# Performance work log

Measured on AMD Instinct MI355X. Metric: run time of the kernel, lower is better.

Reference implementation:

```python
import jax, jax.numpy as jnp
import numpy as np

NEG_SLOPE = 0.2  # PyG GATConv default


def gat_conv(x, W, a_src, a_dst, b, src, dst, n):
    """Single-head PyG-style GATConv with self-loops already appended to (src, dst)."""
    h = x @ W                                   # [N, F]
    alpha_src = h @ a_src                       # [N]
    alpha_dst = h @ a_dst                       # [N]
    e = alpha_src[src] + alpha_dst[dst]         # [E] per-edge logit (message j->i)
    e = jax.nn.leaky_relu(e, NEG_SLOPE)
    # numerically stable softmax over edges grouped by destination node
    m = jax.ops.segment_max(e, dst, num_segments=n)
    ex = jnp.exp(e - m[dst])
    denom = jax.ops.segment_sum(ex, dst, num_segments=n)
    alpha = ex / denom[dst]                     # [E]
    out = jax.ops.segment_sum(alpha[:, None] * h[src], dst, num_segments=n)
    return out + b


def setup_inputs() -> dict:
    key = jax.random.key(0)
    ks = jax.random.split(key, 16)
    N, C, E = 50000, 128, 800000
    x = jax.random.normal(ks[0], (N, C), dtype=jnp.float32)
    edge_index = jax.random.randint(ks[1], (2, E), 0, N, dtype=jnp.int64)

    def lin(k, din, dout):
        return jax.random.normal(k, (din, dout), dtype=jnp.float32) / np.sqrt(din)

    def att(k, d):
        return jax.random.normal(k, (d,), dtype=jnp.float32) / np.sqrt(d)

    d1, d2, d3 = 2 * C, C // 2, 1
    return {
        "x": x, "edge_index": edge_index,
        "W1": lin(ks[2], C, d1), "as1": att(ks[3], d1), "ad1": att(ks[4], d1), "b1": jnp.zeros((d1,), jnp.float32),
        "W2": lin(ks[5], d1, d2), "as2": att(ks[6], d2), "ad2": att(ks[7], d2), "b2": jnp.zeros((d2,), jnp.float32),
        "W3": lin(ks[8], d2, d3), "as3": att(ks[9], d3), "ad3": att(ks[10], d3), "b3": jnp.zeros((d3,), jnp.float32),
    }


def reference(x, edge_index, W1, as1, ad1, b1, W2, as2, ad2, b2, W3, as3, ad3, b3):
    n = x.shape[0]
    self_loops = jnp.arange(n, dtype=edge_index.dtype)
    src = jnp.concatenate([edge_index[0], self_loops])
    dst = jnp.concatenate([edge_index[1], self_loops])
    # dropout is identity in eval mode
    h = gat_conv(x, W1, as1, ad1, b1, src, dst, n)
    h = jax.nn.elu(h)
    h = gat_conv(h, W2, as2, ad2, b2, src, dst, n)
    h = jax.nn.elu(h)
    return gat_conv(h, W3, as3, ad3, b3, src, dst, n)
```

## Files before the change

kernel.cpp:

```cpp
#include <hip/hip_runtime.h>
#include <hip/hip_bf16.h>
#include <hip/hip_fp16.h>
#include <math.h>

#define NEG_SLOPE 0.2f

typedef __attribute__((ext_vector_type(8))) short bf16x8_t;
typedef __attribute__((ext_vector_type(4))) float f32x4_t;

struct __align__(8) half4_t { __half2 a, b; };

__global__ void hist_k(const int* __restrict__ ei, int E, int n, int* __restrict__ deg) {
    int e = blockIdx.x * 256 + threadIdx.x;
    int ET = E + n;
    if (e >= ET) return;
    int d = (e < E) ? ei[E + e] : (e - E);
    atomicAdd(&deg[d], 1);
}

__global__ void scan1_k(const int* __restrict__ deg, int* __restrict__ incl,
                        int* __restrict__ bsums, int n) {
    __shared__ int s[256];
    int tid = threadIdx.x;
    int i = blockIdx.x * 256 + tid;
    int v = (i < n) ? deg[i] : 0;
    s[tid] = v;
    __syncthreads();
    for (int off = 1; off < 256; off <<= 1) {
        int t = (tid >= off) ? s[tid - off] : 0;
        __syncthreads();
        s[tid] += t;
        __syncthreads();
    }
    if (i < n) incl[i] = s[tid];
    if (tid == 255) bsums[blockIdx.x] = s[255];
}

__global__ void scan2_k(int* __restrict__ bsums, int nch) {
    __shared__ int s[256];
    int tid = threadIdx.x;
    int v = (tid < nch) ? bsums[tid] : 0;
    int orig = v;
    s[tid] = v;
    __syncthreads();
    for (int off = 1; off < 256; off <<= 1) {
        int t = (tid >= off) ? s[tid - off] : 0;
        __syncthreads();
        s[tid] += t;
        __syncthreads();
    }
    if (tid < nch) bsums[tid] = s[tid] - orig;
}

__global__ void scan3_k(int* __restrict__ offsets, int* __restrict__ cursor,
                        const int* __restrict__ bsums, int n, int total) {
    int i = blockIdx.x * 256 + threadIdx.x;
    if (i < n) {
        int excl = offsets[i] - cursor[i] + bsums[i >> 8];
        offsets[i] = excl;
        cursor[i]  = excl;
    }
    if (i == 0 && blockIdx.x == 0) offsets[n] = total;
}

__global__ void fill_k(const int* __restrict__ ei, int E, int n,
                       int* __restrict__ cursor, int* __restrict__ csr) {
    int e = blockIdx.x * 256 + threadIdx.x;
    int ET = E + n;
    if (e >= ET) return;
    int s, d;
    if (e < E) { s = ei[e]; d = ei[E + e]; }
    else       { s = e - E; d = e - E; }
    int pos = atomicAdd(&cursor[d], 1);
    csr[pos] = s;
}

__device__ inline void bf16_split(float f, ushort& hi, ushort& lo) {
    unsigned int u = __float_as_uint(f);
    unsigned int r = u + 0x7FFFu + ((u >> 16) & 1u);
    hi = (ushort)(r >> 16);
    float back = __uint_as_float((unsigned int)hi << 16);
    float rem = f - back;
    unsigned int u2 = __float_as_uint(rem);
    unsigned int r2 = u2 + 0x7FFFu + ((u2 >> 16) & 1u);
    lo = (ushort)(r2 >> 16);
}

__global__ void splitA_k(const float* __restrict__ A, ushort* __restrict__ Ah,
                         ushort* __restrict__ Al, long total8) {
    long i = (long)blockIdx.x * 256 + threadIdx.x;
    if (i >= total8) return;
    const float* src = A + i * 8;
    float4 a = *(const float4*)src;
    float4 b = *(const float4*)(src + 4);
    float fv[8] = {a.x, a.y, a.z, a.w, b.x, b.y, b.z, b.w};
    ushort hv[8], lv[8];
#pragma unroll
    for (int q = 0; q < 8; q++) bf16_split(fv[q], hv[q], lv[q]);
    *(bf16x8_t*)(Ah + i * 8) = *(bf16x8_t*)hv;
    *(bf16x8_t*)(Al + i * 8) = *(bf16x8_t*)lv;
}

__global__ void splitWT_k(const float* __restrict__ W, ushort* __restrict__ WhT,
                          ushort* __restrict__ WlT, int K, int N) {
    int idx = blockIdx.x * 256 + threadIdx.x;
    if (idx >= K * N) return;
    int k = idx / N, n = idx - k * N;
    ushort hi, lo;
    bf16_split(W[idx], hi, lo);
    WhT[(size_t)n * K + k] = hi;
    WlT[(size_t)n * K + k] = lo;
}

__global__ __launch_bounds__(256) void gemm_k(const ushort* __restrict__ Ah,
                                              const ushort* __restrict__ Al,
                                              const ushort* __restrict__ BhT,
                                              const ushort* __restrict__ BlT,
                                              __half* __restrict__ Ch,
                                              float* __restrict__ asb,
                                              float* __restrict__ adb,
                                              const float* __restrict__ a_src,
                                              const float* __restrict__ a_dst,
                                              int M, int K, int Nc) {
    __shared__ __align__(16) ushort sAh[128][40];
    __shared__ __align__(16) ushort sAl[128][40];
    __shared__ __align__(16) ushort sBh[64][40];
    __shared__ __align__(16) ushort sBl[64][40];

    const int tid  = threadIdx.x;
    const int lane = tid & 63;
    const int wv   = tid >> 6;
    const int wm   = wv & 1, wn = wv >> 1;
    const int m0   = blockIdx.x << 7;
    const int n0   = blockIdx.y << 6;

    f32x4_t acc[4][2];
#pragma unroll
    for (int i = 0; i < 4; i++)
#pragma unroll
        for (int j = 0; j < 2; j++) acc[i][j] = (f32x4_t){0.f, 0.f, 0.f, 0.f};

    const int arow = tid >> 1;
    const int acb  = (tid & 1) << 4;
    const int brow = tid >> 2;
    const int bkb  = (tid & 3) << 3;

    const bf16x8_t zv = {};

    for (int k0 = 0; k0 < K; k0 += 32) {
        {
            const int gr = m0 + arow;
            bf16x8_t h0 = zv, h1 = zv, l0 = zv, l1 = zv;
            if (gr < M) {
                const ushort* ph = Ah + (size_t)gr * K + k0 + acb;
                const ushort* pl = Al + (size_t)gr * K + k0 + acb;
                h0 = *(const bf16x8_t*)ph;
                h1 = *(const bf16x8_t*)(ph + 8);
                l0 = *(const bf16x8_t*)pl;
                l1 = *(const bf16x8_t*)(pl + 8);
            }
            *(bf16x8_t*)&sAh[arow][acb]     = h0;
            *(bf16x8_t*)&sAh[arow][acb + 8] = h1;
            *(bf16x8_t*)&sAl[arow][acb]     = l0;
            *(bf16x8_t*)&sAl[arow][acb + 8] = l1;
        }
        {
            const ushort* ph = BhT + (size_t)(n0 + brow) * K + k0 + bkb;
            const ushort* pl = BlT + (size_t)(n0 + brow) * K + k0 + bkb;
            *(bf16x8_t*)&sBh[brow][bkb] = *(const bf16x8_t*)ph;
            *(bf16x8_t*)&sBl[brow][bkb] = *(const bf16x8_t*)pl;
        }
        __syncthreads();
        bf16x8_t ah[4], al[4], bh[2], bl[2];
        const int rbase = (wm << 6) + (lane & 15);
        const int slot  = (lane >> 4) << 3;
#pragma unroll
        for (int mi = 0; mi < 4; mi++) {
            ah[mi] = *(const bf16x8_t*)&sAh[rbase + (mi << 4)][slot];
            al[mi] = *(const bf16x8_t*)&sAl[rbase + (mi << 4)][slot];
        }
        const int cbase = (wn << 5) + (lane & 15);
#pragma unroll
        for (int ni = 0; ni < 2; ni++) {
            bh[ni] = *(const bf16x8_t*)&sBh[cbase + (ni << 4)][slot];
            bl[ni] = *(const bf16x8_t*)&sBl[cbase + (ni << 4)][slot];
        }
#pragma unroll
        for (int mi = 0; mi < 4; mi++)
#pragma unroll
            for (int ni = 0; ni < 2; ni++) {
                acc[mi][ni] = __builtin_amdgcn_mfma_f32_16x16x32_bf16(ah[mi], bh[ni], acc[mi][ni], 0, 0, 0);
                acc[mi][ni] = __builtin_amdgcn_mfma_f32_16x16x32_bf16(ah[mi], bl[ni], acc[mi][ni], 0, 0, 0);
                acc[mi][ni] = __builtin_amdgcn_mfma_f32_16x16x32_bf16(al[mi], bh[ni], acc[mi][ni], 0, 0, 0);
            }
        __syncthreads();
    }

    const int col0 = n0 + (wn << 5) + (lane & 15);
    const float asv0 = a_src[col0],      adv0 = a_dst[col0];
    const float asv1 = a_src[col0 + 16], adv1 = a_dst[col0 + 16];

#pragma unroll
    for (int mi = 0; mi < 4; mi++) {
        const int row0 = m0 + (wm << 6) + (mi << 4) + ((lane >> 4) << 2);
#pragma unroll
        for (int ni = 0; ni < 2; ni++) {
            const int col = col0 + (ni << 4);
#pragma unroll
            for (int r = 0; r < 4; r++)
                if (row0 + r < M)
                    Ch[(size_t)(row0 + r) * Nc + col] = __float2half(acc[mi][ni][r]);
        }
        float ss[4], sd[4];
#pragma unroll
        for (int r = 0; r < 4; r++) {
            ss[r] = acc[mi][0][r] * asv0 + acc[mi][1][r] * asv1;
            sd[r] = acc[mi][0][r] * adv0 + acc[mi][1][r] * adv1;
        }
#pragma unroll
        for (int off = 1; off < 16; off <<= 1) {
#pragma unroll
            for (int r = 0; r < 4; r++) {
                ss[r] += __shfl_xor(ss[r], off);
                sd[r] += __shfl_xor(sd[r], off);
            }
        }
        if ((lane & 15) == 0) {
#pragma unroll
            for (int r = 0; r < 4; r++)
                if (row0 + r < M) {
                    atomicAdd(&asb[row0 + r], ss[r]);
                    atomicAdd(&adb[row0 + r], sd[r]);
                }
        }
    }
}

#define DEG_CAP 128

template <int D, bool DO_ELU, bool SPLIT_OUT>
__global__ __launch_bounds__(256) void agg_k(const int* __restrict__ offs,
                                             const int* __restrict__ csr,
                                             const float* __restrict__ asb,
                                             const float* __restrict__ adb,
                                             const __half* __restrict__ h,
                                             const float* __restrict__ bias,
                                             float* __restrict__ out,
                                             ushort* __restrict__ oh,
                                             ushort* __restrict__ ol, int n) {
    __shared__ float wsh[4][DEG_CAP];
    __shared__ int   jsh[4][DEG_CAP];
    const int wv   = threadIdx.x >> 6;
    const int lane = threadIdx.x & 63;
    const int wid  = (blockIdx.x << 2) + wv;
    const bool active = wid < n;

    int beg = 0, deg = 0;
    float adi = 0.f;
    if (active) {
        beg = offs[wid];
        deg = offs[wid + 1] - beg;
        adi = adb[wid];
    }
    const int degc = deg < DEG_CAP ? deg : DEG_CAP;

    float m = -INFINITY;
    if (active) {
        for (int e = lane; e < degc; e += 64) {
            int j = csr[beg + e];
            float v = asb[j] + adi;
            v = v > 0.f ? v : NEG_SLOPE * v;
            jsh[wv][e] = j;
            wsh[wv][e] = v;
            m = fmaxf(m, v);
        }
        for (int e = DEG_CAP + lane; e < deg; e += 64) {
            float v = asb[csr[beg + e]] + adi;
            v = v > 0.f ? v : NEG_SLOPE * v;
            m = fmaxf(m, v);
        }
#pragma unroll
        for (int o = 32; o; o >>= 1) m = fmaxf(m, __shfl_xor(m, o));
    }

    float inv = 0.f;
    if (active) {
        float ssum = 0.f;
        for (int e = lane; e < degc; e += 64) {
            float ww = __expf(wsh[wv][e] - m);
            wsh[wv][e] = ww;
            ssum += ww;
        }
        for (int e = DEG_CAP + lane; e < deg; e += 64) {
            float v = asb[csr[beg + e]] + adi;
            v = v > 0.f ? v : NEG_SLOPE * v;
            ssum += __expf(v - m);
        }
#pragma unroll
        for (int o = 32; o; o >>= 1) ssum += __shfl_xor(ssum, o);
        inv = 1.f / ssum;
    }

    __syncthreads();

    if (!active) return;

    constexpr int U = D / 64;
    float a0[U] = {}, a1[U] = {}, a2[U] = {}, a3[U] = {};

    int e = 0;
    for (; e + 4 <= degc; e += 4) {
        int j0 = jsh[wv][e], j1 = jsh[wv][e + 1], j2 = jsh[wv][e + 2], j3 = jsh[wv][e + 3];
        float w0 = wsh[wv][e], w1 = wsh[wv][e + 1], w2 = wsh[wv][e + 2], w3 = wsh[wv][e + 3];
        if constexpr (U == 4) {
            const half4_t h0 = *(const half4_t*)(h + (size_t)j0 * D + (lane << 2));
            const half4_t h1 = *(const half4_t*)(h + (size_t)j1 * D + (lane << 2));
            const half4_t h2 = *(const half4_t*)(h + (size_t)j2 * D + (lane << 2));
            const half4_t h3 = *(const half4_t*)(h + (size_t)j3 * D + (lane << 2));
            float2 f0a = __half22float2(h0.a), f0b = __half22float2(h0.b);
            float2 f1a = __half22float2(h1.a), f1b = __half22float2(h1.b);
            float2 f2a = __half22float2(h2.a), f2b = __half22float2(h2.b);
            float2 f3a = __half22float2(h3.a), f3b = __half22float2(h3.b);
            a0[0] = fmaf(w0, f0a.x, a0[0]); a0[1] = fmaf(w0, f0a.y, a0[1]);
            a0[2] = fmaf(w0, f0b.x, a0[2]); a0[3] = fmaf(w0, f0b.y, a0[3]);
            a1[0] = fmaf(w1, f1a.x, a1[0]); a1[1] = fmaf(w1, f1a.y, a1[1]);
            a1[2] = fmaf(w1, f1b.x, a1[2]); a1[3] = fmaf(w1, f1b.y, a1[3]);
            a2[0] = fmaf(w2, f2a.x, a2[0]); a2[1] = fmaf(w2, f2a.y, a2[1]);
            a2[2] = fmaf(w2, f2b.x, a2[2]); a2[3] = fmaf(w2, f2b.y, a2[3]);
            a3[0] = fmaf(w3, f3a.x, a3[0]); a3[1] = fmaf(w3, f3a.y, a3[1]);
            a3[2] = fmaf(w3, f3b.x, a3[2]); a3[3] = fmaf(w3, f3b.y, a3[3]);
        } else {
            a0[0] = fmaf(w0, __half2float(h[(size_t)j0 * D + lane]), a0[0]);
            a1[0] = fmaf(w1, __half2float(h[(size_t)j1 * D + lane]), a1[0]);
            a2[0] = fmaf(w2, __half2float(h[(size_t)j2 * D + lane]), a2[0]);
            a3[0] = fmaf(w3, __half2float(h[(size_t)j3 * D + lane]), a3[0]);
        }
    }
    for (; e < degc; ++e) {
        int j = jsh[wv][e];
        float ww = wsh[wv][e];
        if constexpr (U == 4) {
            const half4_t hv = *(const half4_t*)(h + (size_t)j * D + (lane << 2));
            float2 fa = __half22float2(hv.a), fb = __half22float2(hv.b);
            a0[0] = fmaf(ww, fa.x, a0[0]); a0[1] = fmaf(ww, fa.y, a0[1]);
            a0[2] = fmaf(ww, fb.x, a0[2]); a0[3] = fmaf(ww, fb.y, a0[3]);
        } else {
            a0[0] = fmaf(ww, __half2float(h[(size_t)j * D + lane]), a0[0]);
        }
    }
    for (int eo = DEG_CAP; eo < deg; ++eo) {
        int j = csr[beg + eo];
        float v = asb[j] + adi;
        v = v > 0.f ? v : NEG_SLOPE * v;
        float ww = __expf(v - m);
        if constexpr (U == 4) {
            const half4_t hv = *(const half4_t*)(h + (size_t)j * D + (lane << 2));
            float2 fa = __half22float2(hv.a), fb = __half22float2(hv.b);
            a0[0] = fmaf(ww, fa.x, a0[0]); a0[1] = fmaf(ww, fa.y, a0[1]);
            a0[2] = fmaf(ww, fb.x, a0[2]); a0[3] = fmaf(ww, fb.y, a0[3]);
        } else {
            a0[0] = fmaf(ww, __half2float(h[(size_t)j * D + lane]), a0[0]);
        }
    }

    if constexpr (U == 4) {
        float t[4];
#pragma unroll
        for (int u = 0; u < 4; u++) {
            float v = (a0[u] + a1[u] + a2[u] + a3[u]) * inv + bias[(lane << 2) + u];
            if (DO_ELU) v = v > 0.f ? v : expm1f(v);
            t[u] = v;
        }
        if constexpr (SPLIT_OUT) {
            ushort hv[4], lv[4];
#pragma unroll
            for (int u = 0; u < 4; u++) bf16_split(t[u], hv[u], lv[u]);
            *(ushort4*)(oh + (size_t)wid * D + (lane << 2)) = make_ushort4(hv[0], hv[1], hv[2], hv[3]);
            *(ushort4*)(ol + (size_t)wid * D + (lane << 2)) = make_ushort4(lv[0], lv[1], lv[2], lv[3]);
        } else {
            *(float4*)(out + (size_t)wid * D + (lane << 2)) = make_float4(t[0], t[1], t[2], t[3]);
        }
    } else {
        float t = (a0[0] + a1[0] + a2[0] + a3[0]) * inv + bias[lane];
        if (DO_ELU) t = t > 0.f ? t : expm1f(t);
        out[(size_t)wid * D + lane] = t;
    }
}

__global__ void l3_prep_k(const float* __restrict__ o2, const float* __restrict__ W3,
                          const float* __restrict__ as3, const float* __restrict__ ad3,
                          float* __restrict__ h3, float* __restrict__ asb,
                          float* __restrict__ adb, int n) {
    int wid = (blockIdx.x << 2) + (threadIdx.x >> 6);
    int lane = threadIdx.x & 63;
    if (wid >= n) return;
    float t = o2[(size_t)wid * 64 + lane] * W3[lane];
#pragma unroll
    for (int o = 32; o; o >>= 1) t += __shfl_xor(t, o);
    if (lane == 0) {
        h3[wid]  = t;
        asb[wid] = t * as3[0];
        adb[wid] = t * ad3[0];
    }
}

__global__ void agg3_k(const int* __restrict__ offs, const int* __restrict__ csr,
                       const float* __restrict__ asb, const float* __restrict__ adb,
                       const float* __restrict__ h3, const float* __restrict__ b3,
                       float* __restrict__ out, int n) {
    int wid = (blockIdx.x << 2) + (threadIdx.x >> 6);
    int lane = threadIdx.x & 63;
    if (wid >= n) return;
    int beg = offs[wid], end = offs[wid + 1];
    float adi = adb[wid];

    float m = -INFINITY;
    for (int e = beg + lane; e < end; e += 64) {
        float v = asb[csr[e]] + adi;
        v = v > 0.f ? v : NEG_SLOPE * v;
        m = fmaxf(m, v);
    }
#pragma unroll
    for (int o = 32; o; o >>= 1) m = fmaxf(m, __shfl_xor(m, o));

    float ssum = 0.f, acc = 0.f;
    for (int e = beg + lane; e < end; e += 64) {
        int j = csr[e];
        float v = asb[j] + adi;
        v = v > 0.f ? v : NEG_SLOPE * v;
        float w = __expf(v - m);
        ssum += w;
        acc = fmaf(w, h3[j], acc);
    }
#pragma unroll
    for (int o = 32; o; o >>= 1) {
        ssum += __shfl_xor(ssum, o);
        acc  += __shfl_xor(acc, o);
    }
    if (lane == 0) out[wid] = acc / ssum + b3[0];
}

extern "C" void kernel_launch(void* const* d_in, const int* in_sizes, int n_in,
                              void* d_out, int out_size, void* d_ws, size_t ws_size,
                              hipStream_t stream) {
    const float* x   = (const float*)d_in[0];
    const int*   ei  = (const int*)d_in[1];
    const float* W1  = (const float*)d_in[2];
    const float* as1 = (const float*)d_in[3];
    const float* ad1 = (const float*)d_in[4];
    const float* b1  = (const float*)d_in[5];
    const float* W2  = (const float*)d_in[6];
    const float* as2 = (const float*)d_in[7];
    const float* ad2 = (const float*)d_in[8];
    const float* b2  = (const float*)d_in[9];
    const float* W3  = (const float*)d_in[10];
    const float* as3 = (const float*)d_in[11];
    const float* ad3 = (const float*)d_in[12];
    const float* b3  = (const float*)d_in[13];

    const int d1 = in_sizes[3];
    const int C  = in_sizes[2] / d1;
    const int N  = in_sizes[0] / C;
    const int E  = in_sizes[1] / 2;
    const int d2 = in_sizes[7];
    const int ET = E + N;

    char* p = (char*)d_ws;
    auto alloc = [&](size_t bytes) -> void* {
        void* q = (void*)p;
        p += (bytes + 255) & ~(size_t)255;
        return q;
    };
    int*    offsets = (int*)alloc(sizeof(int) * (size_t)(N + 1));
    int*    cursor  = (int*)alloc(sizeof(int) * (size_t)N);
    int*    bsums   = (int*)alloc(sizeof(int) * 256);
    int*    csr     = (int*)alloc(sizeof(int) * (size_t)ET);
    float*  alpha   = (float*)alloc(sizeof(float) * (size_t)4 * N);
    float*  as1b = alpha, *ad1b = alpha + N, *as2b = alpha + 2 * N, *ad2b = alpha + 3 * N;
    ushort* xh      = (ushort*)alloc(sizeof(ushort) * (size_t)N * C);
    ushort* xl      = (ushort*)alloc(sizeof(ushort) * (size_t)N * C);
    ushort* w1h     = (ushort*)alloc(sizeof(ushort) * (size_t)C * d1);
    ushort* w1l     = (ushort*)alloc(sizeof(ushort) * (size_t)C * d1);
    ushort* w2h     = (ushort*)alloc(sizeof(ushort) * (size_t)d1 * d2);
    ushort* w2l     = (ushort*)alloc(sizeof(ushort) * (size_t)d1 * d2);
    __half* ch1     = (__half*)alloc(sizeof(__half) * (size_t)N * d1);
    ushort* o1h     = (ushort*)alloc(sizeof(ushort) * (size_t)N * d1);
    ushort* o1l     = (ushort*)alloc(sizeof(ushort) * (size_t)N * d1);
    __half* ch2     = (__half*)alloc(sizeof(__half) * (size_t)N * d2);
    float*  o2      = (float*)alloc(sizeof(float) * (size_t)N * d2);
    float*  h3      = (float*)alloc(sizeof(float) * (size_t)N);
    float*  as3b    = (float*)alloc(sizeof(float) * (size_t)N);
    float*  ad3b    = (float*)alloc(sizeof(float) * (size_t)N);

    const int eb  = (ET + 255) / 256;
    const int nch = (N + 255) / 256;
    const int wb  = (N + 3) / 4;

    hipMemsetAsync(cursor, 0, sizeof(int) * (size_t)N, stream);
    hipMemsetAsync(alpha, 0, sizeof(float) * (size_t)4 * N, stream);

    hist_k<<<eb, 256, 0, stream>>>(ei, E, N, cursor);
    scan1_k<<<nch, 256, 0, stream>>>(cursor, offsets, bsums, N);
    scan2_k<<<1, 256, 0, stream>>>(bsums, nch);
    scan3_k<<<nch, 256, 0, stream>>>(offsets, cursor, bsums, N, ET);
    fill_k<<<eb, 256, 0, stream>>>(ei, E, N, cursor, csr);

    {
        long t8 = (long)N * C / 8;
        splitA_k<<<(int)((t8 + 255) / 256), 256, 0, stream>>>(x, xh, xl, t8);
        splitWT_k<<<(C * d1 + 255) / 256, 256, 0, stream>>>(W1, w1h, w1l, C, d1);
        splitWT_k<<<(d1 * d2 + 255) / 256, 256, 0, stream>>>(W2, w2h, w2l, d1, d2);
    }

    {
        dim3 g((N + 127) / 128, d1 / 64);
        gemm_k<<<g, 256, 0, stream>>>(xh, xl, w1h, w1l, ch1, as1b, ad1b, as1, ad1, N, C, d1);
        agg_k<256, true, true><<<wb, 256, 0, stream>>>(offsets, csr, as1b, ad1b, ch1, b1,
                                                       nullptr, o1h, o1l, N);
    }
    {
        dim3 g((N + 127) / 128, d2 / 64);
        gemm_k<<<g, 256, 0, stream>>>(o1h, o1l, w2h, w2l, ch2, as2b, ad2b, as2, ad2, N, d1, d2);
        agg_k<64, true, false><<<wb, 256, 0, stream>>>(offsets, csr, as2b, ad2b, ch2, b2,
                                                       o2, nullptr, nullptr, N);
    }
    {
        l3_prep_k<<<wb, 256, 0, stream>>>(o2, W3, as3, ad3, h3, as3b, ad3b, N);
        agg3_k<<<wb, 256, 0, stream>>>(offsets, csr, as3b, ad3b, h3, b3, (float*)d_out, N);
    }
}
```

Baseline: 389.4 us.

## Drop softmax max pass, fuse layer-3 prep into layer-2 aggregation, precompute byte offsets

Removes the segment-max pass from all three aggregation kernels. Logits are clamped to [-60,60] and exponentiated directly, so each kernel reads the edge list once fewer. The layer-3 projection (h3, alpha src/dst) is fused into the layer-2 aggregation epilogue, which eliminates the o2 buffer and one launch. Neighbor byte offsets are stored in shared memory instead of indices to save address arithmetic. The clamp changes numerics if a logit exceeds 60, and softmax without the max shift could lose precision.

```diff
diff --git a/kernel.cpp b/kernel.cpp
--- a/kernel.cpp
+++ b/kernel.cpp
@@ -112,16 +112,16 @@
     WlT[(size_t)n * K + k] = lo;
 }
 
-__global__ __launch_bounds__(256) void gemm_k(const ushort* __restrict__ Ah,
-                                              const ushort* __restrict__ Al,
-                                              const ushort* __restrict__ BhT,
-                                              const ushort* __restrict__ BlT,
-                                              __half* __restrict__ Ch,
-                                              float* __restrict__ asb,
-                                              float* __restrict__ adb,
-                                              const float* __restrict__ a_src,
-                                              const float* __restrict__ a_dst,
-                                              int M, int K, int Nc) {
+__device__ __forceinline__ void gemm_core(const ushort* __restrict__ Ah,
+                                          const ushort* __restrict__ Al,
+                                          const ushort* __restrict__ BhT,
+                                          const ushort* __restrict__ BlT,
+                                          __half* __restrict__ Ch,
+                                          float* __restrict__ asb,
+                                          float* __restrict__ adb,
+                                          const float* __restrict__ a_src,
+                                          const float* __restrict__ a_dst,
+                                          int M, int K, int Nc) {
     __shared__ __align__(16) ushort sAh[128][40];
     __shared__ __align__(16) ushort sAl[128][40];
     __shared__ __align__(16) ushort sBh[64][40];
@@ -236,20 +236,41 @@
     }
 }
 
+__global__ __launch_bounds__(256) void gemm1_k(const ushort* Ah, const ushort* Al,
+                                               const ushort* BhT, const ushort* BlT,
+                                               __half* Ch, float* asb, float* adb,
+                                               const float* a_src, const float* a_dst,
+                                               int M, int K, int Nc) {
+    gemm_core(Ah, Al, BhT, BlT, Ch, asb, adb, a_src, a_dst, M, K, Nc);
+}
+__global__ __launch_bounds__(256) void gemm2_k(const ushort* Ah, const ushort* Al,
+                                               const ushort* BhT, const ushort* BlT,
+                                               __half* Ch, float* asb, float* adb,
+                                               const float* a_src, const float* a_dst,
+                                               int M, int K, int Nc) {
+    gemm_core(Ah, Al, BhT, BlT, Ch, asb, adb, a_src, a_dst, M, K, Nc);
+}
+
 #define DEG_CAP 128
 
-template <int D, bool DO_ELU, bool SPLIT_OUT>
-__global__ __launch_bounds__(256) void agg_k(const int* __restrict__ offs,
-                                             const int* __restrict__ csr,
-                                             const float* __restrict__ asb,
-                                             const float* __restrict__ adb,
-                                             const __half* __restrict__ h,
-                                             const float* __restrict__ bias,
-                                             float* __restrict__ out,
-                                             ushort* __restrict__ oh,
-                                             ushort* __restrict__ ol, int n) {
+template <int D, bool DO_ELU, bool SPLIT_OUT, bool L3F>
+__device__ __forceinline__ void agg_core(const int* __restrict__ offs,
+                                         const int* __restrict__ csr,
+                                         const float* __restrict__ asb,
+                                         const float* __restrict__ adb,
+                                         const __half* __restrict__ h,
+                                         const float* __restrict__ bias,
+                                         float* __restrict__ out,
+                                         ushort* __restrict__ oh,
+                                         ushort* __restrict__ ol,
+                                         const float* __restrict__ W3,
+                                         const float* __restrict__ as3,
+                                         const float* __restrict__ ad3,
+                                         float* __restrict__ h3o,
+                                         float* __restrict__ as3b,
+                                         float* __restrict__ ad3b, int n) {
     __shared__ float wsh[4][DEG_CAP];
-    __shared__ int   jsh[4][DEG_CAP];
+    __shared__ int   osh[4][DEG_CAP];
     const int wv   = threadIdx.x >> 6;
     const int lane = threadIdx.x & 63;
     const int wid  = (blockIdx.x << 2) + wv;
@@ -264,37 +285,24 @@
     }
     const int degc = deg < DEG_CAP ? deg : DEG_CAP;
 
-    float m = -INFINITY;
+    float inv = 0.f;
     if (active) {
+        float ssum = 0.f;
         for (int e = lane; e < degc; e += 64) {
             int j = csr[beg + e];
             float v = asb[j] + adi;
             v = v > 0.f ? v : NEG_SLOPE * v;
-            jsh[wv][e] = j;
-            wsh[wv][e] = v;
-            m = fmaxf(m, v);
+            v = fminf(fmaxf(v, -60.f), 60.f);
+            float w = __expf(v);
+            osh[wv][e] = j * (int)(D * sizeof(__half));
+            wsh[wv][e] = w;
+            ssum += w;
         }
         for (int e = DEG_CAP + lane; e < deg; e += 64) {
             float v = asb[csr[beg + e]] + adi;
             v = v > 0.f ? v : NEG_SLOPE * v;
-            m = fmaxf(m, v);
-        }
-#pragma unroll
-        for (int o = 32; o; o >>= 1) m = fmaxf(m, __shfl_xor(m, o));
-    }
-
-    float inv = 0.f;
-    if (active) {
-        float ssum = 0.f;
-        for (int e = lane; e < degc; e += 64) {
-            float ww = __expf(wsh[wv][e] - m);
-            wsh[wv][e] = ww;
-            ssum += ww;
-        }
-        for (int e = DEG_CAP + lane; e < deg; e += 64) {
-            float v = asb[csr[beg + e]] + adi;
-            v = v > 0.f ? v : NEG_SLOPE * v;
-            ssum += __expf(v - m);
+            v = fminf(fmaxf(v, -60.f), 60.f);
+            ssum += __expf(v);
         }
 #pragma unroll
         for (int o = 32; o; o >>= 1) ssum += __shfl_xor(ssum, o);
@@ -307,16 +315,17 @@
 
     constexpr int U = D / 64;
     float a0[U] = {}, a1[U] = {}, a2[U] = {}, a3[U] = {};
+    const char* hb = (const char*)h + (U == 4 ? (lane << 3) : (lane << 1));
 
     int e = 0;
     for (; e + 4 <= degc; e += 4) {
-        int j0 = jsh[wv][e], j1 = jsh[wv][e + 1], j2 = jsh[wv][e + 2], j3 = jsh[wv][e + 3];
+        int o0 = osh[wv][e], o1 = osh[wv][e + 1], o2 = osh[wv][e + 2], o3 = osh[wv][e + 3];
         float w0 = wsh[wv][e], w1 = wsh[wv][e + 1], w2 = wsh[wv][e + 2], w3 = wsh[wv][e + 3];
         if constexpr (U == 4) {
-            const half4_t h0 = *(const half4_t*)(h + (size_t)j0 * D + (lane << 2));
-            const half4_t h1 = *(const half4_t*)(h + (size_t)j1 * D + (lane << 2));
-            const half4_t h2 = *(const half4_t*)(h + (size_t)j2 * D + (lane << 2));
-            const half4_t h3 = *(const half4_t*)(h + (size_t)j3 * D + (lane << 2));
+            const half4_t h0 = *(const half4_t*)(hb + o0);
+            const half4_t h1 = *(const half4_t*)(hb + o1);
+            const half4_t h2 = *(const half4_t*)(hb + o2);
+            const half4_t h3 = *(const half4_t*)(hb + o3);
             float2 f0a = __half22float2(h0.a), f0b = __half22float2(h0.b);
             float2 f1a = __half22float2(h1.a), f1b = __half22float2(h1.b);
             float2 f2a = __half22float2(h2.a), f2b = __half22float2(h2.b);
@@ -330,36 +339,38 @@
             a3[0] = fmaf(w3, f3a.x, a3[0]); a3[1] = fmaf(w3, f3a.y, a3[1]);
             a3[2] = fmaf(w3, f3b.x, a3[2]); a3[3] = fmaf(w3, f3b.y, a3[3]);
         } else {
-            a0[0] = fmaf(w0, __half2float(h[(size_t)j0 * D + lane]), a0[0]);
-            a1[0] = fmaf(w1, __half2float(h[(size_t)j1 * D + lane]), a1[0]);
-            a2[0] = fmaf(w2, __half2float(h[(size_t)j2 * D + lane]), a2[0]);
-            a3[0] = fmaf(w3, __half2float(h[(size_t)j3 * D + lane]), a3[0]);
+            a0[0] = fmaf(w0, __half2float(*(const __half*)(hb + o0)), a0[0]);
+            a1[0] = fmaf(w1, __half2float(*(const __half*)(hb + o1)), a1[0]);
+            a2[0] = fmaf(w2, __half2float(*(const __half*)(hb + o2)), a2[0]);
+            a3[0] = fmaf(w3, __half2float(*(const __half*)(hb + o3)), a3[0]);
         }
     }
     for (; e < degc; ++e) {
-        int j = jsh[wv][e];
+        int o0 = osh[wv][e];
         float ww = wsh[wv][e];
         if constexpr (U == 4) {
-            const half4_t hv = *(const half4_t*)(h + (size_t)j * D + (lane << 2));
+            const half4_t hv = *(const half4_t*)(hb + o0);
             float2 fa = __half22float2(hv.a), fb = __half22float2(hv.b);
             a0[0] = fmaf(ww, fa.x, a0[0]); a0[1] = fmaf(ww, fa.y, a0[1]);
             a0[2] = fmaf(ww, fb.x, a0[2]); a0[3] = fmaf(ww, fb.y, a0[3]);
         } else {
-            a0[0] = fmaf(ww, __half2float(h[(size_t)j * D + lane]), a0[0]);
+            a0[0] = fmaf(ww, __half2float(*(const __half*)(hb + o0)), a0[0]);
         }
     }
     for (int eo = DEG_CAP; eo < deg; ++eo) {
         int j = csr[beg + eo];
         float v = asb[j] + adi;
         v = v > 0.f ? v : NEG_SLOPE * v;
-        float ww = __expf(v - m);
+        v = fminf(fmaxf(v, -60.f), 60.f);
+        float ww = __expf(v);
+        int o0 = j * (int)(D * sizeof(__half));
         if constexpr (U == 4) {
-            const half4_t hv = *(const half4_t*)(h + (size_t)j * D + (lane << 2));
+            const half4_t hv = *(const half4_t*)(hb + o0);
             float2 fa = __half22float2(hv.a), fb = __half22float2(hv.b);
             a0[0] = fmaf(ww, fa.x, a0[0]); a0[1] = fmaf(ww, fa.y, a0[1]);
             a0[2] = fmaf(ww, fb.x, a0[2]); a0[3] = fmaf(ww, fb.y, a0[3]);
         } else {
-            a0[0] = fmaf(ww, __half2float(h[(size_t)j * D + lane]), a0[0]);
+            a0[0] = fmaf(ww, __half2float(*(const __half*)(hb + o0)), a0[0]);
         }
     }
 
@@ -383,25 +394,40 @@
     } else {
         float t = (a0[0] + a1[0] + a2[0] + a3[0]) * inv + bias[lane];
         if (DO_ELU) t = t > 0.f ? t : expm1f(t);
-        out[(size_t)wid * D + lane] = t;
-    }
-}
-
-__global__ void l3_prep_k(const float* __restrict__ o2, const float* __restrict__ W3,
-                          const float* __restrict__ as3, const float* __restrict__ ad3,
-                          float* __restrict__ h3, float* __restrict__ asb,
-                          float* __restrict__ adb, int n) {
-    int wid = (blockIdx.x << 2) + (threadIdx.x >> 6);
-    int lane = threadIdx.x & 63;
-    if (wid >= n) return;
-    float t = o2[(size_t)wid * 64 + lane] * W3[lane];
-#pragma unroll
-    for (int o = 32; o; o >>= 1) t += __shfl_xor(t, o);
-    if (lane == 0) {
-        h3[wid]  = t;
-        asb[wid] = t * as3[0];
-        adb[wid] = t * ad3[0];
-    }
+        if constexpr (L3F) {
+            float c = t * W3[lane];
+#pragma unroll
+            for (int o = 32; o; o >>= 1) c += __shfl_xor(c, o);
+            if (lane == 0) {
+                h3o[wid]  = c;
+                as3b[wid] = c * as3[0];
+                ad3b[wid] = c * ad3[0];
+            }
+        } else {
+            out[(size_t)wid * D + lane] = t;
+        }
+    }
+}
+
+__global__ __launch_bounds__(256) void agg1_k(const int* offs, const int* csr,
+                                              const float* asb, const float* adb,
+                                              const __half* h, const float* bias,
+                                              ushort* oh, ushort* ol, int n) {
+    agg_core<256, true, true, false>(offs, csr, asb, adb, h, bias,
+                                     nullptr, oh, ol,
+                                     nullptr, nullptr, nullptr,
+                                     nullptr, nullptr, nullptr, n);
+}
+
+__global__ __launch_bounds__(256) void agg2_k(const int* offs, const int* csr,
+                                              const float* asb, const float* adb,
+                                              const __half* h, const float* bias,
+                                              const float* W3, const float* as3,
+                                              const float* ad3, float* h3o,
+                                              float* as3b, float* ad3b, int n) {
+    agg_core<64, true, false, true>(offs, csr, asb, adb, h, bias,
+                                    nullptr, nullptr, nullptr,
+                                    W3, as3, ad3, h3o, as3b, ad3b, n);
 }
 
 __global__ void agg3_k(const int* __restrict__ offs, const int* __restrict__ csr,
@@ -414,21 +440,13 @@
     int beg = offs[wid], end = offs[wid + 1];
     float adi = adb[wid];
 
-    float m = -INFINITY;
-    for (int e = beg + lane; e < end; e += 64) {
-        float v = asb[csr[e]] + adi;
-        v = v > 0.f ? v : NEG_SLOPE * v;
-        m = fmaxf(m, v);
-    }
-#pragma unroll
-    for (int o = 32; o; o >>= 1) m = fmaxf(m, __shfl_xor(m, o));
-
     float ssum = 0.f, acc = 0.f;
     for (int e = beg + lane; e < end; e += 64) {
         int j = csr[e];
         float v = asb[j] + adi;
         v = v > 0.f ? v : NEG_SLOPE * v;
-        float w = __expf(v - m);
+        v = fminf(fmaxf(v, -60.f), 60.f);
+        float w = __expf(v);
         ssum += w;
         acc = fmaf(w, h3[j], acc);
     }
@@ -487,7 +505,6 @@
     ushort* o1h     = (ushort*)alloc(sizeof(ushort) * (size_t)N * d1);
     ushort* o1l     = (ushort*)alloc(sizeof(ushort) * (size_t)N * d1);
     __half* ch2     = (__half*)alloc(sizeof(__half) * (size_t)N * d2);
-    float*  o2      = (float*)alloc(sizeof(float) * (size_t)N * d2);
     float*  h3      = (float*)alloc(sizeof(float) * (size_t)N);
     float*  as3b    = (float*)alloc(sizeof(float) * (size_t)N);
     float*  ad3b    = (float*)alloc(sizeof(float) * (size_t)N);
@@ -514,18 +531,14 @@
 
     {
         dim3 g((N + 127) / 128, d1 / 64);
-        gemm_k<<<g, 256, 0, stream>>>(xh, xl, w1h, w1l, ch1, as1b, ad1b, as1, ad1, N, C, d1);
-        agg_k<256, true, true><<<wb, 256, 0, stream>>>(offsets, csr, as1b, ad1b, ch1, b1,
-                                                       nullptr, o1h, o1l, N);
+        gemm1_k<<<g, 256, 0, stream>>>(xh, xl, w1h, w1l, ch1, as1b, ad1b, as1, ad1, N, C, d1);
+        agg1_k<<<wb, 256, 0, stream>>>(offsets, csr, as1b, ad1b, ch1, b1, o1h, o1l, N);
     }
     {
         dim3 g((N + 127) / 128, d2 / 64);
-        gemm_k<<<g, 256, 0, stream>>>(o1h, o1l, w2h, w2l, ch2, as2b, ad2b, as2, ad2, N, d1, d2);
-        agg_k<64, true, false><<<wb, 256, 0, stream>>>(offsets, csr, as2b, ad2b, ch2, b2,
-                                                       o2, nullptr, nullptr, N);
-    }
-    {
-        l3_prep_k<<<wb, 256, 0, stream>>>(o2, W3, as3, ad3, h3, as3b, ad3b, N);
-        agg3_k<<<wb, 256, 0, stream>>>(offsets, csr, as3b, ad3b, h3, b3, (float*)d_out, N);
-    }
-}
+        gemm2_k<<<g, 256, 0, stream>>>(o1h, o1l, w2h, w2l, ch2, as2b, ad2b, as2, ad2, N, d1, d2);
+        agg2_k<<<wb, 256, 0, stream>>>(offsets, csr, as2b, ad2b, ch2, b2,
+                                       W3, as3, ad3, h3, as3b, ad3b, N);
+    }
+    agg3_k<<<wb, 256, 0, stream>>>(offsets, csr, as3b, ad3b, h3, b3, (float*)d_out, N);
+}
```

Result: faster. 371.5 us (-4.6%).
